# Kernel optimization log

Hardware: AMD Instinct MI355X
Metric: run time of the kernel (lower is better)

The kernel has to match this reference:

```python
import jax, jax.numpy as jnp
import numpy as np

GAMMA = 1.0  # get_gamma(1, None) == 1


def setup_inputs() -> dict:
    key = jax.random.key(0)
    # scale down so recursion divisors 1 - km^2 stay well-conditioned
    a = jax.random.normal(key, (2048, 1024, 33), dtype=jnp.float32) * 0.05
    return {"a": a}


def reference(a):
    # LPC -> PARCOR (reverse Levinson-Durbin recursion), a: [..., M+1]
    M = a.shape[-1] - 1
    K = a[..., :1]          # gain term, passed through
    ar = a[..., 1:] * GAMMA  # working LPC coefficients, length M
    ks = []
    # Python loop over the (small, fixed) LPC order; fully vectorized over batch.
    for m in range(M - 1, -1, -1):
        km = ar[..., m:m + 1]           # reflection coefficient k_m
        ks.append(km)
        if m == 0:
            break
        z = 1.0 - km * km
        k = ar[..., :m]                 # step-down: shrink order by one
        ar = (k - km * k[..., ::-1]) / z
    ks.append(K)
    return jnp.concatenate(ks[::-1], axis=-1)
```

## Files before the change

kernel.cpp:

```cpp
#include <hip/hip_runtime.h>

#define M 32
#define NC 33
#define TPB 128
#define FPB (TPB * NC)
#define V4 8
#define TAIL (V4 * 4 * TPB)
#define NBLOCKS 2048

typedef float f4 __attribute__((ext_vector_type(4)));

__device__ __forceinline__ void levinson(float* __restrict__ lds, int rb) {
    float ar[M];
#pragma unroll
    for (int j = 0; j < M; ++j) ar[j] = lds[rb + 1 + j];
#pragma unroll
    for (int m = M - 1; m >= 1; --m) {
        float km = ar[m];
        lds[rb + m + 1] = km;
        float z = 1.0f - km * km;
        float r = 1.0f / z;
        const int h = m >> 1;
#pragma unroll
        for (int j = 0; j < h; ++j) {
            float x = ar[j], y = ar[m - 1 - j];
            ar[j]         = (x - km * y) * r;
            ar[m - 1 - j] = (y - km * x) * r;
        }
        if (m & 1) ar[h] = (ar[h] - km * ar[h]) * r;
    }
    lds[rb + 1] = ar[0];
}

__device__ __forceinline__ void store_tile_nt(float* __restrict__ dst,
                                              const float* __restrict__ lds, int t) {
    const f4* l4 = (const f4*)lds;
#pragma unroll
    for (int k = 0; k < V4; ++k) {
        f4 v = l4[t + k * TPB];
        __builtin_nontemporal_store(v, (f4*)dst + t + k * TPB);
    }
    __builtin_nontemporal_store(lds[TAIL + t], dst + TAIL + t);
}

__device__ __forceinline__ void process_tile_guarded(float* __restrict__ lds,
                                                     const float* __restrict__ a,
                                                     float* __restrict__ out,
                                                     long long base, long long limit, int t) {
    for (int k = 0; k < NC; ++k) {
        int g = t + k * TPB;
        long long ga = base + g;
        lds[g] = (ga < limit) ? a[ga] : 0.0f;
    }
    __syncthreads();
    levinson(lds, t * NC);
    __syncthreads();
    for (int k = 0; k < NC; ++k) {
        int g = t + k * TPB;
        long long ga = base + g;
        if (ga < limit) out[ga] = lds[g];
    }
    __syncthreads();
}

__global__ __launch_bounds__(TPB)
void lpc_to_parcor_kernel(const float* __restrict__ a,
                          float* __restrict__ out,
                          long long nrows, long long tiles_per_block) {
    __shared__ float lds[FPB];
    const int t = threadIdx.x;
    const long long limit = nrows * NC;
    const long long ntiles = (nrows + TPB - 1) / TPB;
    const long long nfull  = nrows / TPB;

    long long t0 = (long long)blockIdx.x * tiles_per_block;
    long long t1 = t0 + tiles_per_block; if (t1 > ntiles) t1 = ntiles;
    if (t0 >= t1) return;
    long long fend = (t1 < nfull) ? t1 : nfull;

    if (t0 < fend) {
        f4 p[V4]; float pt;
        {
            const float* src = a + t0 * FPB;
            const f4* s4 = (const f4*)src;
#pragma unroll
            for (int k = 0; k < V4; ++k) p[k] = s4[t + k * TPB];
            pt = src[TAIL + t];
        }
        for (long long ti = t0; ti < fend; ++ti) {
            {
                f4* l4 = (f4*)lds;
#pragma unroll
                for (int k = 0; k < V4; ++k) l4[t + k * TPB] = p[k];
                lds[TAIL + t] = pt;
            }
            __syncthreads();

            if (ti + 1 < fend) {
                const float* src = a + (ti + 1) * FPB;
                const f4* s4 = (const f4*)src;
#pragma unroll
                for (int k = 0; k < V4; ++k) p[k] = s4[t + k * TPB];
                pt = src[TAIL + t];
            }
            __builtin_amdgcn_sched_barrier(0);

            levinson(lds, t * NC);
            __syncthreads();

            store_tile_nt(out + ti * FPB, lds, t);
        }
    }
    for (long long ti = (t0 > nfull ? t0 : nfull); ti < t1; ++ti) {
        __syncthreads();
        process_tile_guarded(lds, a, out, ti * FPB, limit, t);
    }
}

extern "C" void kernel_launch(void* const* d_in, const int* in_sizes, int n_in,
                              void* d_out, int out_size, void* d_ws, size_t ws_size,
                              hipStream_t stream) {
    const float* a = (const float*)d_in[0];
    float* out = (float*)d_out;
    long long nrows = (long long)in_sizes[0] / NC;
    long long ntiles = (nrows + TPB - 1) / TPB;
    long long blocks = (ntiles < NBLOCKS) ? ntiles : NBLOCKS;
    long long tpb_tiles = (ntiles + blocks - 1) / blocks;
    lpc_to_parcor_kernel<<<(int)blocks, TPB, 0, stream>>>(a, out, nrows, tpb_tiles);
}
```

Baseline: 102.9 us.

## Double-buffer tiles in LDS via direct global-to-LDS DMA loads

Replaces the register-staged prefetch with global_load_lds DMA into a second LDS buffer. The next tile streams straight into shared memory while the current tile runs the Levinson step-down, synchronised with hand-written vmcnt/lgkmcnt waits and raw barriers. This removes the register round trip and the LDS write pass. In exchange it doubles LDS per block and relies on in-order vmcnt counting that mixes DMA loads with nontemporal stores. The grid is also halved to 1024 blocks.

```diff
diff --git a/kernel.cpp b/kernel.cpp
--- a/kernel.cpp
+++ b/kernel.cpp
@@ -4,11 +4,34 @@
 #define NC 33
 #define TPB 128
 #define FPB (TPB * NC)
+#define TAIL 4096
 #define V4 8
-#define TAIL (V4 * 4 * TPB)
-#define NBLOCKS 2048
+#define NBLOCKS 1024
 
 typedef float f4 __attribute__((ext_vector_type(4)));
+
+__device__ __forceinline__ void dma16(const float* g, float* l) {
+    __builtin_amdgcn_global_load_lds(
+        (const __attribute__((address_space(1))) unsigned int*)g,
+        (__attribute__((address_space(3))) unsigned int*)l, 16, 0, 0);
+}
+__device__ __forceinline__ void dma4(const float* g, float* l) {
+    __builtin_amdgcn_global_load_lds(
+        (const __attribute__((address_space(1))) unsigned int*)g,
+        (__attribute__((address_space(3))) unsigned int*)l, 4, 0, 0);
+}
+
+__device__ __forceinline__ void issue_tile_dma(const float* __restrict__ src,
+                                               float* __restrict__ lbuf,
+                                               int w, int lane) {
+#pragma unroll
+    for (int k = 0; k < 8; ++k) {
+        int fi = w * 2048 + k * 256 + lane * 4;
+        dma16(src + fi, lbuf + w * 2048 + k * 256);
+    }
+    int ft = TAIL + w * 64 + lane;
+    dma4(src + ft, lbuf + TAIL + w * 64);
+}
 
 __device__ __forceinline__ void levinson(float* __restrict__ lds, int rb) {
     float ar[M];
@@ -67,8 +90,9 @@
 void lpc_to_parcor_kernel(const float* __restrict__ a,
                           float* __restrict__ out,
                           long long nrows, long long tiles_per_block) {
-    __shared__ float lds[FPB];
+    __shared__ float lds[2 * FPB];
     const int t = threadIdx.x;
+    const int w = t >> 6, lane = t & 63;
     const long long limit = nrows * NC;
     const long long ntiles = (nrows + TPB - 1) / TPB;
     const long long nfull  = nrows / TPB;
@@ -79,36 +103,33 @@
     long long fend = (t1 < nfull) ? t1 : nfull;
 
     if (t0 < fend) {
-        f4 p[V4]; float pt;
-        {
-            const float* src = a + t0 * FPB;
-            const f4* s4 = (const f4*)src;
-#pragma unroll
-            for (int k = 0; k < V4; ++k) p[k] = s4[t + k * TPB];
-            pt = src[TAIL + t];
-        }
+        issue_tile_dma(a + t0 * FPB, lds, w, lane);
+
         for (long long ti = t0; ti < fend; ++ti) {
-            {
-                f4* l4 = (f4*)lds;
-#pragma unroll
-                for (int k = 0; k < V4; ++k) l4[t + k * TPB] = p[k];
-                lds[TAIL + t] = pt;
+            float* cur = lds + ((int)((ti - t0) & 1)) * FPB;
+            float* nxt = lds + ((int)((ti - t0 + 1) & 1)) * FPB;
+            const bool has_next = (ti + 1 < fend);
+
+            if (has_next) issue_tile_dma(a + (ti + 1) * FPB, nxt, w, lane);
+
+            if (ti == t0) {
+                if (has_next) asm volatile("s_waitcnt vmcnt(9)" ::: "memory");
+                else          asm volatile("s_waitcnt vmcnt(0)" ::: "memory");
+            } else {
+                if (has_next) asm volatile("s_waitcnt vmcnt(18)" ::: "memory");
+                else          asm volatile("s_waitcnt vmcnt(9)" ::: "memory");
             }
-            __syncthreads();
+            __builtin_amdgcn_s_barrier();
 
-            if (ti + 1 < fend) {
-                const float* src = a + (ti + 1) * FPB;
-                const f4* s4 = (const f4*)src;
-#pragma unroll
-                for (int k = 0; k < V4; ++k) p[k] = s4[t + k * TPB];
-                pt = src[TAIL + t];
-            }
-            __builtin_amdgcn_sched_barrier(0);
+            levinson(cur, t * NC);
 
-            levinson(lds, t * NC);
-            __syncthreads();
+            asm volatile("s_waitcnt lgkmcnt(0)" ::: "memory");
+            __builtin_amdgcn_s_barrier();
 
-            store_tile_nt(out + ti * FPB, lds, t);
+            store_tile_nt(out + ti * FPB, cur, t);
+
+            asm volatile("s_waitcnt lgkmcnt(0)" ::: "memory");
+            __builtin_amdgcn_s_barrier();
         }
     }
     for (long long ti = (t0 > nfull ? t0 : nfull); ti < t1; ++ti) {
```

Result: slower. 115.4 us (+12.2%).
